# Kernel tuning notes

Measured on AMD Instinct MI355X. Metric: run time of the kernel, lower is better.

The kernel has to match this reference:

```python
import jax, jax.numpy as jnp
import numpy as np

B, H, W, C = 4, 128, 128, 256
HEADS, DHEAD = 8, 32


def conv2d(x, w, b=None, groups=1, pad=0):
    # x: [N,C,H,W], w: [O, C//groups, kh, kw]
    out = jax.lax.conv_general_dilated(
        x, w, window_strides=(1, 1), padding=[(pad, pad), (pad, pad)],
        dimension_numbers=("NCHW", "OIHW", "NCHW"), feature_group_count=groups)
    if b is not None:
        out = out + b[None, :, None, None]
    return out


def setup_inputs() -> dict:
    key = jax.random.key(0)
    ks = jax.random.split(key, 16)
    g = lambda i, shape, s=0.02: jax.random.normal(ks[i], shape, jnp.float32) * s
    return {
        "x": jax.random.normal(ks[0], (B, H, W, C), jnp.float32),
        "mask": jax.random.uniform(ks[1], (1, C, H, W), jnp.float32),
        "wq": g(2, (C, C)),
        "wk": g(3, (C, C)),
        "wv": g(4, (C, C)),
        "rescale": jnp.ones((HEADS, 1, 1), jnp.float32),
        "wproj": g(5, (C, C)),
        "bproj": jnp.zeros((C,), jnp.float32),
        "mg_w1": g(6, (C, C, 1, 1)),
        "mg_b1": jnp.zeros((C,), jnp.float32),
        "mg_w2": g(7, (C, C, 1, 1)),
        "mg_b2": jnp.zeros((C,), jnp.float32),
        "mg_dw": g(8, (C, 1, 5, 5)),
        "mg_db": jnp.zeros((C,), jnp.float32),
        "be_w1": g(9, (C, 1, 3, 3)),
        "be_w2": g(10, (C, 1, 3, 3)),
    }


def _l2norm(t, axis):
    n = jnp.sqrt(jnp.sum(t * t, axis=axis, keepdims=True))
    return t / jnp.maximum(n, 1e-12)


def reference(x, mask, wq, wk, wv, rescale, wproj, bproj,
              mg_w1, mg_b1, mg_w2, mg_b2, mg_dw, mg_db, be_w1, be_w2):
    b, h, w, c = x.shape
    heads = rescale.shape[0]
    d = c // heads
    n = h * w

    xf = x.reshape(b, n, c)
    q_inp = xf @ wq   # [b,n,c]
    k_inp = xf @ wk
    v_inp = xf @ wv

    # MaskGuidedMechanism (h==w so shift_back is identity)
    m = conv2d(mask, mg_w1, mg_b1)                                   # [1,c,h,w]
    attn_map = jax.nn.sigmoid(conv2d(conv2d(m, mg_w2, mg_b2), mg_dw, mg_db, groups=c, pad=2))
    m = m * attn_map + m
    mask_emb = jnp.transpose(m, (0, 2, 3, 1))                        # [1,h,w,c]
    ma = jnp.broadcast_to(mask_emb, (b, h, w, c)).reshape(b, n, c)

    split = lambda t: t.reshape(b, n, heads, d).transpose(0, 2, 1, 3)  # [b,heads,n,d]
    q, k, v, ma = map(split, (q_inp, k_inp, v_inp, ma))
    v = v * ma

    # channel attention: normalize over token dim n
    qn = _l2norm(q, axis=2)
    kn = _l2norm(k, axis=2)
    attn = jnp.einsum("bhni,bhnj->bhij", kn, qn)                     # [b,heads,d,d]
    attn = jax.nn.softmax(attn * rescale, axis=-1)
    out = jnp.einsum("bhij,bhnj->bhin", attn, v)                     # [b,heads,d,n]

    out = out.transpose(0, 3, 1, 2).reshape(b, n, heads * d)         # [b,n,c]
    out_c = (out @ wproj + bproj).reshape(b, h, w, c)

    # band_emb: depthwise3x3 -> GELU(exact) -> depthwise3x3 on v_inp image
    v_img = v_inp.reshape(b, h, w, c).transpose(0, 3, 1, 2)          # [b,c,h,w]
    y = conv2d(v_img, be_w1, groups=c, pad=1)
    y = jax.nn.gelu(y, approximate=False)
    y = conv2d(y, be_w2, groups=c, pad=1)
    out_p = y.transpose(0, 2, 3, 1)

    return out_c + out_p
```

## Files before the change

### kernel.cpp

```cpp
#include <hip/hip_runtime.h>
#include <stdint.h>

#define B 4
#define HW 128
#define C 256
#define NTOK 16384
#define MALL 65536
#define HEADS 8
#define DH 32

typedef float f32x4 __attribute__((ext_vector_type(4)));
typedef short s16x8 __attribute__((ext_vector_type(8)));
typedef short s16x4 __attribute__((ext_vector_type(4)));
typedef __bf16 bf16x8 __attribute__((ext_vector_type(8)));

__device__ __forceinline__ float bf2f(unsigned short u) {
  union { unsigned int i; float f; } x;
  x.i = ((unsigned int)u) << 16;
  return x.f;
}
__device__ __forceinline__ unsigned short f2bf(float f) {
  union { float f; unsigned int i; } x;
  x.f = f;
  unsigned int lsb = (x.i >> 16) & 1u;
  unsigned int r = x.i + 0x7fffu + lsb;
  return (unsigned short)(r >> 16);
}

__device__ __forceinline__ void gload_lds16(const void* g, void* l) {
  auto gp = reinterpret_cast<const __attribute__((address_space(1))) unsigned int*>(
      reinterpret_cast<uintptr_t>(g));
  auto lp = reinterpret_cast<__attribute__((address_space(3))) unsigned int*>(
      reinterpret_cast<uintptr_t>(l));
  __builtin_amdgcn_global_load_lds(gp, lp, 16, 0, 0);
}

#define CFENCE asm volatile("" ::: "memory")
#define RAWBAR()                      \
  do {                                \
    CFENCE;                           \
    __builtin_amdgcn_s_barrier();     \
    CFENCE;                           \
  } while (0)
#define LDSBAR()                                        \
  do {                                                  \
    asm volatile("s_waitcnt lgkmcnt(0)" ::: "memory");  \
    __builtin_amdgcn_s_barrier();                       \
    CFENCE;                                             \
  } while (0)

__global__ __launch_bounds__(256) void cast_x_kernel(const float* __restrict__ x,
                                                     unsigned short* __restrict__ xb) {
  const size_t stride = (size_t)gridDim.x * blockDim.x * 4;
  for (size_t i = ((size_t)blockIdx.x * blockDim.x + threadIdx.x) * 4; i < (size_t)MALL * C;
       i += stride) {
    const float4 v = *(const float4*)&x[i];
    s16x4 o;
    o[0] = (short)f2bf(v.x);
    o[1] = (short)f2bf(v.y);
    o[2] = (short)f2bf(v.z);
    o[3] = (short)f2bf(v.w);
    *(s16x4*)&xb[i] = o;
  }
}

__global__ __launch_bounds__(256) void prep_w_kernel(
    const float* __restrict__ wq, const float* __restrict__ wk, const float* __restrict__ wv,
    const float* __restrict__ wproj, const float* __restrict__ w1, const float* __restrict__ w2,
    unsigned short* __restrict__ wqkvT, unsigned short* __restrict__ wprojT,
    unsigned short* __restrict__ w1b, unsigned short* __restrict__ w2b) {
  const int idx = blockIdx.x * 256 + threadIdx.x;
  const int mat = blockIdx.y;
  const int n = idx >> 8, k = idx & 255;
  switch (mat) {
    case 0: wqkvT[idx] = f2bf(wq[k * 256 + n]); break;
    case 1: wqkvT[65536 + idx] = f2bf(wk[k * 256 + n]); break;
    case 2: wqkvT[131072 + idx] = f2bf(wv[k * 256 + n]); break;
    case 3: wprojT[idx] = f2bf(wproj[k * 256 + n]); break;
    case 4: w1b[idx] = f2bf(w1[idx]); break;
    case 5: w2b[idx] = f2bf(w2[idx]); break;
  }
}

__global__ __launch_bounds__(1024) void tmask_kernel(const float* __restrict__ mask,
                                                     unsigned short* __restrict__ mT) {
  __shared__ float tile[32][33];
  const int p0 = blockIdx.x * 32, c0 = blockIdx.y * 32;
  const int tx = threadIdx.x & 31, ty = threadIdx.x >> 5;
  tile[ty][tx] = mask[(size_t)(c0 + ty) * NTOK + p0 + tx];
  __syncthreads();
  mT[(size_t)(p0 + ty) * C + c0 + tx] = f2bf(tile[tx][ty]);
}

__global__ __launch_bounds__(512) void gemm_bt256_kernel(
    const unsigned short* __restrict__ A, const unsigned short* __restrict__ Bt,
    const int nbn, const int mode, unsigned short* __restrict__ ob0,
    unsigned short* __restrict__ ob1, unsigned short* __restrict__ ob2,
    const float* __restrict__ bias, float* __restrict__ of32,
    const unsigned short* __restrict__ y2) {
  __shared__ alignas(16) unsigned short smem[32768];
  unsigned short* lAb = smem;
  unsigned short* lBb = smem + 16384;
  const int nwg = gridDim.x;
  const int bid = blockIdx.x;
  const int qd = nwg >> 3, rr = nwg & 7;
  const int xcd = bid & 7, sidx = bid >> 3;
  const int swz = (xcd < rr ? xcd * (qd + 1) : rr * (qd + 1) + (xcd - rr) * qd) + sidx;
  const int m0 = (swz / nbn) * 256;
  const int n0 = (swz % nbn) * 256;
  const int t = threadIdx.x;
  const int w = t >> 6, l = t & 63;
  const int wr = w >> 2, wc = w & 3;
  const int lr = l & 15, lg = l >> 4;

  const int srow = t >> 2;
  const int ssl = (t & 3) ^ ((t >> 3) & 3);

  auto stageA = [&](int kt) {
    unsigned short* d = lAb + (kt & 1) * 8192;
    const size_t kb = ((size_t)kt * 32 + ssl * 8) * 2;
    gload_lds16((const char*)A + ((size_t)(m0 + srow) * 256) * 2 + kb, (char*)d + t * 16);
    gload_lds16((const char*)A + ((size_t)(m0 + 128 + srow) * 256) * 2 + kb,
                (char*)d + 8192 + t * 16);
  };
  auto stageB = [&](int kt) {
    unsigned short* d = lBb + (kt & 1) * 8192;
    const size_t kb = ((size_t)kt * 32 + ssl * 8) * 2;
    gload_lds16((const char*)Bt + ((size_t)(n0 + srow) * 256) * 2 + kb, (char*)d + t * 16);
    gload_lds16((const char*)Bt + ((size_t)(n0 + 128 + srow) * 256) * 2 + kb,
                (char*)d + 8192 + t * 16);
  };

  f32x4 acc[8][4];
#pragma unroll
  for (int m = 0; m < 8; ++m)
#pragma unroll
    for (int j = 0; j < 4; ++j) acc[m][j] = f32x4{0.f, 0.f, 0.f, 0.f};

  const int asl = (lg ^ ((lr >> 1) & 3)) * 8;
  const int aoff = lr * 32 + asl;
  const int awb = wr * 4096;
  const int boff = (wc >> 1) * 4096 + ((wc & 1) * 64 + lr) * 32 + asl;

  stageA(0); stageB(0);
  asm volatile("s_waitcnt vmcnt(0)" ::: "memory");
  RAWBAR();

#pragma unroll
  for (int kt = 0; kt < 8; ++kt) {
    const unsigned short* bufA = lAb + (kt & 1) * 8192;
    const unsigned short* bufB = lBb + (kt & 1) * 8192;
    bf16x8 bfr[4], af[4], af2[4];
#pragma unroll
    for (int j = 0; j < 4; ++j) bfr[j] = *(const bf16x8*)&bufB[boff + j * 512];
#pragma unroll
    for (int m = 0; m < 4; ++m) af[m] = *(const bf16x8*)&bufA[awb + aoff + m * 512];
#pragma unroll
    for (int m = 0; m < 4; ++m) af2[m] = *(const bf16x8*)&bufA[awb + aoff + (m + 4) * 512];
    if (kt < 7) { stageA(kt + 1); stageB(kt + 1); }
    __builtin_amdgcn_s_setprio(1);
#pragma unroll
    for (int m = 0; m < 4; ++m)
#pragma unroll
      for (int j = 0; j < 4; ++j)
        acc[m][j] = __builtin_amdgcn_mfma_f32_16x16x32_bf16(af[m], bfr[j], acc[m][j], 0, 0, 0);
#pragma unroll
    for (int m = 0; m < 4; ++m)
#pragma unroll
      for (int j = 0; j < 4; ++j)
        acc[m + 4][j] =
            __builtin_amdgcn_mfma_f32_16x16x32_bf16(af2[m], bfr[j], acc[m + 4][j], 0, 0, 0);
    __builtin_amdgcn_s_setprio(0);
    if (kt < 7) asm volatile("s_waitcnt vmcnt(0)" ::: "memory");
    RAWBAR();
  }

  if (mode == 0) {
    unsigned short* dst = (n0 < 256) ? ob0 : (n0 < 512 ? ob1 : ob2);
    unsigned short* eph = smem;
#pragma unroll
    for (int c = 0; c < 4; ++c) {
      LDSBAR();
      if (wr == (c >> 1)) {
#pragma unroll
        for (int mm = 0; mm < 4; ++mm) {
          const int m = (c & 1) * 4 + mm;
          const int lrow = mm * 16 + lg * 4;
#pragma unroll
          for (int j = 0; j < 4; ++j) {
            const int col = wc * 64 + j * 16 + lr;
#pragma unroll
            for (int r = 0; r < 4; ++r) eph[(lrow + r) * 264 + col] = f2bf(acc[m][j][r]);
          }
        }
      }
      LDSBAR();
      const int col16 = t & 31;
#pragma unroll
      for (int c2 = 0; c2 < 4; ++c2) {
        const int lrow = c2 * 16 + (t >> 5);
        const int grow = m0 + c * 64 + lrow;
        const s16x8 v = *(const s16x8*)&eph[lrow * 264 + col16 * 8];
        *(s16x8*)&dst[(size_t)grow * C + col16 * 8] = v;
      }
    }
  } else {
    float* ephf = (float*)smem;
    const int colc = t & 63;
    const f32x4 bv = *(const f32x4*)&bias[colc * 4];
#pragma unroll
    for (int c = 0; c < 8; ++c) {
      LDSBAR();
      if (wr == (c >> 2)) {
#pragma unroll
        for (int mm = 0; mm < 2; ++mm) {
          const int m = (c & 3) * 2 + mm;
          const int lrow = mm * 16 + lg * 4;
#pragma unroll
          for (int j = 0; j < 4; ++j) {
            const int col = wc * 64 + j * 16 + lr;
#pragma unroll
            for (int r = 0; r < 4; ++r) ephf[(lrow + r) * 260 + col] = acc[m][j][r];
          }
        }
      }
      LDSBAR();
#pragma unroll
      for (int c2 = 0; c2 < 4; ++c2) {
        const int lrow = c2 * 8 + (t >> 6);
        const int grow = m0 + c * 32 + lrow;
        const f32x4 v = *(const f32x4*)&ephf[lrow * 260 + colc * 4];
        const s16x4 yv = *(const s16x4*)&y2[(size_t)grow * C + colc * 4];
        f32x4 o;
#pragma unroll
        for (int e = 0; e < 4; ++e) o[e] = v[e] + bv[e] + bf2f((unsigned short)yv[e]);
        *(f32x4*)&of32[(size_t)grow * C + colc * 4] = o;
      }
    }
  }
}

__global__ __launch_bounds__(256) void gemm_bt_kernel(
    const unsigned short* __restrict__ A, const unsigned short* __restrict__ Bt, const int K,
    const int nbn, const int mode, unsigned short* __restrict__ ob0,
    unsigned short* __restrict__ ob1, unsigned short* __restrict__ ob2,
    const float* __restrict__ bias, float* __restrict__ of32) {
  __shared__ unsigned short lA[2][128 * 64];
  __shared__ unsigned short lB[2][128 * 64];
  const int nwg = gridDim.x;
  const int bid = blockIdx.x;
  const int qd = nwg >> 3, rr = nwg & 7;
  const int xcd = bid & 7, sidx = bid >> 3;
  const int swz = (xcd < rr ? xcd * (qd + 1) : rr * (qd + 1) + (xcd - rr) * qd) + sidx;
  const int m0 = (swz / nbn) * 128;
  const int n0 = (swz % nbn) * 128;
  const int t = threadIdx.x;
  const int w = t >> 6, l = t & 63;
  const int wr = w >> 1, wc = w & 1;
  const int lr = l & 15, lg = l >> 4;

  const int strow = (l >> 3);
  const int scolb = (((l & 7) ^ strow) << 4);

  f32x4 acc[4][4];
#pragma unroll
  for (int i = 0; i < 4; ++i)
#pragma unroll
    for (int j = 0; j < 4; ++j) acc[i][j] = f32x4{0.f, 0.f, 0.f, 0.f};

  auto stage = [&](int buf, int k0) {
#pragma unroll
    for (int s = 0; s < 4; ++s) {
      const int seg = w * 4 + s;
      const int row = seg * 8 + strow;
      gload_lds16((const char*)A + ((size_t)(m0 + row) * K + k0) * 2 + scolb,
                  (char*)&lA[buf][0] + seg * 1024 + (l & 7) * 16);
      gload_lds16((const char*)Bt + ((size_t)(n0 + row) * K + k0) * 2 + scolb,
                  (char*)&lB[buf][0] + seg * 1024 + (l & 7) * 16);
    }
  };
  auto compute = [&](int buf) {
#pragma unroll
    for (int kk = 0; kk < 64; kk += 32) {
      bf16x8 af[4], bfr[4];
      const int sbase = (kk >> 3) + lg;
      const int p = (sbase ^ (lr & 7)) << 3;
#pragma unroll
      for (int i = 0; i < 4; ++i)
        af[i] = *(const bf16x8*)&lA[buf][(wr * 64 + i * 16 + lr) * 64 + p];
#pragma unroll
      for (int j = 0; j < 4; ++j)
        bfr[j] = *(const bf16x8*)&lB[buf][(wc * 64 + j * 16 + lr) * 64 + p];
#pragma unroll
      for (int i = 0; i < 4; ++i)
#pragma unroll
        for (int j = 0; j < 4; ++j)
          acc[i][j] = __builtin_amdgcn_mfma_f32_16x16x32_bf16(af[i], bfr[j], acc[i][j], 0, 0, 0);
    }
  };

  stage(0, 0);
  __syncthreads();
  int cur = 0;
  for (int k0 = 64; k0 < K; k0 += 64) {
    stage(cur ^ 1, k0);
    compute(cur);
    __syncthreads();
    cur ^= 1;
  }
  compute(cur);

#pragma unroll
  for (int i = 0; i < 4; ++i) {
    const int grow = m0 + wr * 64 + i * 16 + lg * 4;
#pragma unroll
    for (int j = 0; j < 4; ++j) {
      const int gcol = n0 + wc * 64 + j * 16 + lr;
#pragma unroll
      for (int r = 0; r < 4; ++r) {
        const float v = acc[i][j][r];
        const size_t row = (size_t)(grow + r);
        if (mode == 0) {
          unsigned short* dst = (gcol < 256) ? ob0 : (gcol < 512 ? ob1 : ob2);
          dst[row * C + (gcol & 255)] = f2bf(v);
        } else if (mode == 1) {
          ob0[row * C + gcol] = f2bf(v + bias[gcol]);
        } else {
          const size_t idx = row * C + gcol;
          of32[idx] += v + bias[gcol];
        }
      }
    }
  }
}

__global__ __launch_bounds__(256) void mask_dw5_kernel(
    const unsigned short* __restrict__ m2, const unsigned short* __restrict__ m1,
    const float* __restrict__ dw, const float* __restrict__ db,
    unsigned short* __restrict__ memb) {
  __shared__ float wlds[25 * 256];
  __shared__ float blds[256];
  const int t = threadIdx.x;
  const int y = blockIdx.y;
  const int x0 = blockIdx.x * 16 + (t >> 6) * 4;
  const int cg = (t & 63) * 4;
#pragma unroll
  for (int e = 0; e < 25; ++e) wlds[e * 256 + t] = dw[t * 25 + e];
  blds[t] = db[t];
  __syncthreads();

  const f32x4 bias = *(const f32x4*)&blds[cg];
  f32x4 acc[4];
#pragma unroll
  for (int xi = 0; xi < 4; ++xi) acc[xi] = bias;

#pragma unroll
  for (int dy = 0; dy < 5; ++dy) {
    const int yy = y + dy - 2;
    if (yy < 0 || yy >= HW) continue;
    f32x4 col[8];
#pragma unroll
    for (int j = 0; j < 8; ++j) {
      const int xx = x0 - 2 + j;
      if (xx >= 0 && xx < HW) {
        const s16x4 v = *(const s16x4*)&m2[((size_t)yy * HW + xx) * C + cg];
        col[j][0] = bf2f((unsigned short)v[0]);
        col[j][1] = bf2f((unsigned short)v[1]);
        col[j][2] = bf2f((unsigned short)v[2]);
        col[j][3] = bf2f((unsigned short)v[3]);
      } else {
        col[j] = f32x4{0.f, 0.f, 0.f, 0.f};
      }
    }
#pragma unroll
    for (int dx = 0; dx < 5; ++dx) {
      const f32x4 wv = *(const f32x4*)&wlds[(dy * 5 + dx) * 256 + cg];
#pragma unroll
      for (int xi = 0; xi < 4; ++xi) acc[xi] += wv * col[dx + xi];
    }
  }

#pragma unroll
  for (int xi = 0; xi < 4; ++xi) {
    const size_t oi = ((size_t)y * HW + x0 + xi) * C + cg;
    const s16x4 mv = *(const s16x4*)&m1[oi];
    s16x4 o;
#pragma unroll
    for (int ch = 0; ch < 4; ++ch) {
      const float a = 1.f / (1.f + __expf(-acc[xi][ch]));
      o[ch] = (short)f2bf(bf2f((unsigned short)mv[ch]) * (1.f + a));
    }
    *(s16x4*)&memb[oi] = o;
  }
}

__global__ __launch_bounds__(256) void gram_kernel(const unsigned short* __restrict__ qb,
                                                   const unsigned short* __restrict__ kb,
                                                   float* __restrict__ Gpart,
                                                   float* __restrict__ ssq,
                                                   float* __restrict__ ssk) {
  const int chunk = blockIdx.x;
  const int h = blockIdx.y;
  const int b = blockIdx.z;
  __shared__ unsigned short lk[128 * 32], lq[128 * 32];
  const int t = threadIdx.x;
  const int wv = t >> 6;
  const int i0 = (t & 7) * 4, j0 = ((t >> 3) & 7) * 4;
  const int lrow = t >> 2, lcb = (t & 3) * 8;
  float acc[4][4] = {};
  float sq[8] = {}, sk[8] = {};
  for (int sub = 0; sub < 8; ++sub) {
    const size_t nbase = (size_t)b * NTOK + chunk * 1024 + sub * 128;
    __syncthreads();
#pragma unroll
    for (int it = 0; it < 2; ++it) {
      const int row = it * 64 + lrow;
      const s16x8 kv8 = *(const s16x8*)&kb[(nbase + row) * C + h * 32 + lcb];
      const s16x8 qv8 = *(const s16x8*)&qb[(nbase + row) * C + h * 32 + lcb];
      *(s16x8*)&lk[row * 32 + lcb] = kv8;
      *(s16x8*)&lq[row * 32 + lcb] = qv8;
#pragma unroll
      for (int e = 0; e < 8; ++e) {
        const float kf = bf2f((unsigned short)kv8[e]);
        sk[e] += kf * kf;
        const float qf = bf2f((unsigned short)qv8[e]);
        sq[e] += qf * qf;
      }
    }
    __syncthreads();
    for (int n = wv; n < 128; n += 4) {
      s16x4 kv = *(const s16x4*)&lk[n * 32 + i0];
      s16x4 qv = *(const s16x4*)&lq[n * 32 + j0];
      float kf[4], qf[4];
#pragma unroll
      for (int e = 0; e < 4; ++e) {
        kf[e] = bf2f((unsigned short)kv[e]);
        qf[e] = bf2f((unsigned short)qv[e]);
      }
#pragma unroll
      for (int a = 0; a < 4; ++a)
#pragma unroll
        for (int bb = 0; bb < 4; ++bb) acc[a][bb] += kf[a] * qf[bb];
    }
  }
  const int pc = chunk * 4 + wv;
  float* dst = Gpart + (((size_t)pc * B + b) * HEADS + h) * 1024;
#pragma unroll
  for (int a = 0; a < 4; ++a)
#pragma unroll
    for (int bb = 0; bb < 4; ++bb) dst[(i0 + a) * 32 + (j0 + bb)] = acc[a][bb];
  __syncthreads();
  float* fq = (float*)lq;
  float* fk = (float*)lk;
#pragma unroll
  for (int e = 0; e < 8; ++e) {
    fq[t * 8 + e] = sq[e];
    fk[t * 8 + e] = sk[e];
  }
  __syncthreads();
  if (t < 32) {
    const int tm = t >> 3, e = t & 7;
    float s1 = 0.f, s2 = 0.f;
    for (int k2 = 0; k2 < 64; ++k2) {
      const int tt = tm + k2 * 4;
      s1 += fq[tt * 8 + e];
      s2 += fk[tt * 8 + e];
    }
    ssq[((size_t)b * 16 + chunk) * C + h * 32 + t] = s1;
    ssk[((size_t)b * 16 + chunk) * C + h * 32 + t] = s2;
  }
}

__global__ __launch_bounds__(256) void softmax_kernel(
    const float* __restrict__ Gpart, const float* __restrict__ ssq,
    const float* __restrict__ ssk, const float* __restrict__ rescale,
    unsigned short* __restrict__ attnb) {
  const int h = blockIdx.x, b = blockIdx.y;
  const int t = threadIdx.x;
  __shared__ float G[1024];
  __shared__ float nq[32], nk[32];
#pragma unroll
  for (int e = 0; e < 4; ++e) {
    const int cell = e * 256 + t;
    float s = 0.f;
    for (int pc = 0; pc < 64; ++pc)
      s += Gpart[(((size_t)pc * B + b) * HEADS + h) * 1024 + cell];
    G[cell] = s;
  }
  if (t < 64) {
    const int d = t & 31;
    const float* ss = (t < 32) ? ssq : ssk;
    float s = 0.f;
    for (int ch = 0; ch < 16; ++ch) s += ss[((size_t)b * 16 + ch) * C + h * 32 + d];
    const float nn = fmaxf(sqrtf(s), 1e-12f);
    if (t < 32) nq[d] = nn;
    else nk[d] = nn;
  }
  __syncthreads();
  if (t < 32) {
    const int i = t;
    const float rs = rescale[h];
    float row[32];
    float mx = -1e30f;
#pragma unroll
    for (int j = 0; j < 32; ++j) {
      const float v = G[i * 32 + j] / (nk[i] * nq[j]) * rs;
      row[j] = v;
      mx = fmaxf(mx, v);
    }
    float sum = 0.f;
#pragma unroll
    for (int j = 0; j < 32; ++j) {
      const float e = expf(row[j] - mx);
      row[j] = e;
      sum += e;
    }
    const float inv = 1.f / sum;
#pragma unroll
    for (int j = 0; j < 32; ++j)
      attnb[(((size_t)b * HEADS + h) * 32 + i) * 32 + j] = f2bf(row[j] * inv);
  }
}

#define PVP 264
#define ATP 40
__global__ __launch_bounds__(256) void pv_kernel(const unsigned short* __restrict__ vb,
                                                 const unsigned short* __restrict__ memb,
                                                 const unsigned short* __restrict__ attnb,
                                                 unsigned short* __restrict__ outp) {
  const int n0 = blockIdx.x * 64;
  const int b = blockIdx.y;
  __shared__ unsigned short vma[64 * PVP];
  __shared__ unsigned short at[HEADS * 32 * ATP];
  const int t = threadIdx.x, w = t >> 6, l = t & 63;
  const int lr = l & 15, lg = l >> 4;
  for (int e = t; e < 8192; e += 256) {
    const int h = e >> 10, ij = e & 1023;
    at[(h * 32 + (ij >> 5)) * ATP + (ij & 31)] = attnb[(size_t)b * 8192 + e];
  }
  {
    const int row = t >> 2, cs = (t & 3) * 64;
#pragma unroll
    for (int i2 = 0; i2 < 8; ++i2) {
      const int c = cs + i2 * 8;
      s16x8 vv = *(const s16x8*)&vb[((size_t)b * NTOK + n0 + row) * C + c];
      s16x8 mm = *(const s16x8*)&memb[(size_t)(n0 + row) * C + c];
      s16x8 o;
#pragma unroll
      for (int e = 0; e < 8; ++e)
        o[e] = (short)f2bf(bf2f((unsigned short)vv[e]) * bf2f((unsigned short)mm[e]));
      *(s16x8*)&vma[row * PVP + c] = o;
    }
  }
  __syncthreads();
  f32x4 acc[4][4];
#pragma unroll
  for (int i = 0; i < 4; ++i)
#pragma unroll
    for (int j = 0; j < 4; ++j) acc[i][j] = f32x4{0.f, 0.f, 0.f, 0.f};
#pragma unroll
  for (int j = 0; j < 4; ++j) {
    const int head = w * 2 + (j >> 1);
    const int colh = (j & 1) * 16 + lr;
    const bf16x8 bfr = *(const bf16x8*)&at[(head * 32 + colh) * ATP + lg * 8];
#pragma unroll
    for (int i = 0; i < 4; ++i) {
      const bf16x8 af = *(const bf16x8*)&vma[(i * 16 + lr) * PVP + head * 32 + lg * 8];
      acc[i][j] = __builtin_amdgcn_mfma_f32_16x16x32_bf16(af, bfr, acc[i][j], 0, 0, 0);
    }
  }
#pragma unroll
  for (int i = 0; i < 4; ++i) {
#pragma unroll
    for (int j = 0; j < 4; ++j) {
      const int head = w * 2 + (j >> 1);
      const int gcol = head * 32 + (j & 1) * 16 + lr;
      const int grow = n0 + i * 16 + lg * 4;
#pragma unroll
      for (int r = 0; r < 4; ++r)
        outp[((size_t)b * NTOK + grow + r) * C + gcol] = f2bf(acc[i][j][r]);
    }
  }
}

__global__ __launch_bounds__(512) void dw3_kernel(const unsigned short* __restrict__ in,
                                                  const float* __restrict__ wgt,
                                                  unsigned short* __restrict__ out_bf,
                                                  float* __restrict__ out_f32,
                                                  const int do_gelu, const int write_f32) {
  const int y = blockIdx.x;
  const int b = blockIdx.y;
  const int t = threadIdx.x;
  const int cg = (t & 63) * 4;
  const int x0 = (t >> 6) * 16;
  float w[9][4];
#pragma unroll
  for (int e = 0; e < 9; ++e)
#pragma unroll
    for (int ch = 0; ch < 4; ++ch) w[e][ch] = wgt[(cg + ch) * 9 + e];
  const int ym = y - 1, yp = y + 1;
  const bool hm = (ym >= 0), hp = (yp < HW);
  const size_t base = (size_t)b * NTOK * C + cg;
  auto ld4 = [&](int yy, int xx) -> f32x4 {
    const s16x4 v = *(const s16x4*)&in[base + ((size_t)yy * HW + xx) * C];
    f32x4 f;
    f[0] = bf2f((unsigned short)v[0]);
    f[1] = bf2f((unsigned short)v[1]);
    f[2] = bf2f((unsigned short)v[2]);
    f[3] = bf2f((unsigned short)v[3]);
    return f;
  };
  const f32x4 zero = {0.f, 0.f, 0.f, 0.f};
  f32x4 a0, a1, a2, b0, b1, b2;
  if (x0 > 0) {
    a0 = hm ? ld4(ym, x0 - 1) : zero;
    a1 = ld4(y, x0 - 1);
    a2 = hp ? ld4(yp, x0 - 1) : zero;
  } else {
    a0 = a1 = a2 = zero;
  }
  b0 = hm ? ld4(ym, x0) : zero;
  b1 = ld4(y, x0);
  b2 = hp ? ld4(yp, x0) : zero;
  for (int xi = 0; xi < 16; ++xi) {
    const int x = x0 + xi;
    f32x4 c0, c1, c2;
    if (x + 1 < HW) {
      c0 = hm ? ld4(ym, x + 1) : zero;
      c1 = ld4(y, x + 1);
      c2 = hp ? ld4(yp, x + 1) : zero;
    } else {
      c0 = c1 = c2 = zero;
    }
    float res[4];
#pragma unroll
    for (int ch = 0; ch < 4; ++ch) {
      float r = w[0][ch] * a0[ch] + w[1][ch] * b0[ch] + w[2][ch] * c0[ch] +
                w[3][ch] * a1[ch] + w[4][ch] * b1[ch] + w[5][ch] * c1[ch] +
                w[6][ch] * a2[ch] + w[7][ch] * b2[ch] + w[8][ch] * c2[ch];
      if (do_gelu) r = 0.5f * r * (1.f + erff(r * 0.70710678118654752f));
      res[ch] = r;
    }
    const size_t oi = base + ((size_t)y * HW + x) * C;
    if (write_f32) {
      const f32x4 o = {res[0], res[1], res[2], res[3]};
      *(f32x4*)&out_f32[oi] = o;
    } else {
      s16x4 o;
      o[0] = (short)f2bf(res[0]);
      o[1] = (short)f2bf(res[1]);
      o[2] = (short)f2bf(res[2]);
      o[3] = (short)f2bf(res[3]);
      *(s16x4*)&out_bf[oi] = o;
    }
    a0 = b0; a1 = b1; a2 = b2;
    b0 = c0; b1 = c1; b2 = c2;
  }
}

extern "C" void kernel_launch(void* const* d_in, const int* in_sizes, int n_in, void* d_out,
                              int out_size, void* d_ws, size_t ws_size, hipStream_t stream) {
  (void)in_sizes; (void)n_in; (void)out_size; (void)ws_size;
  const float* x = (const float*)d_in[0];
  const float* maskp = (const float*)d_in[1];
  const float* wq = (const float*)d_in[2];
  const float* wk = (const float*)d_in[3];
  const float* wv = (const float*)d_in[4];
  const float* rescale = (const float*)d_in[5];
  const float* wproj = (const float*)d_in[6];
  const float* bproj = (const float*)d_in[7];
  const float* mg_w1 = (const float*)d_in[8];
  const float* mg_b1 = (const float*)d_in[9];
  const float* mg_w2 = (const float*)d_in[10];
  const float* mg_b2 = (const float*)d_in[11];
  const float* mg_dw = (const float*)d_in[12];
  const float* mg_db = (const float*)d_in[13];
  const float* be_w1 = (const float*)d_in[14];
  const float* be_w2 = (const float*)d_in[15];
  float* out = (float*)d_out;
  char* ws = (char*)d_ws;

  unsigned short* xb = (unsigned short*)(ws + 0ull);
  unsigned short* qb = (unsigned short*)(ws + 33554432ull);
  unsigned short* kb = (unsigned short*)(ws + 67108864ull);
  unsigned short* vb = (unsigned short*)(ws + 100663296ull);
  unsigned short* mT = (unsigned short*)(ws + 134217728ull);
  unsigned short* m1b = (unsigned short*)(ws + 142606336ull);
  unsigned short* m2b = (unsigned short*)(ws + 150994944ull);
  unsigned short* wqkvT = (unsigned short*)(ws + 159383552ull);
  unsigned short* wprojT = (unsigned short*)(ws + 159776768ull);
  unsigned short* w1b = (unsigned short*)(ws + 159907840ull);
  unsigned short* w2b = (unsigned short*)(ws + 160038912ull);
  float* ssq = (float*)(ws + 160169984ull);
  float* ssk = (float*)(ws + 160432128ull);
  unsigned short* attnb = (unsigned short*)(ws + 160694272ull);
  float* Gpart = (float*)m2b;
  unsigned short* memb = mT;
  unsigned short* outpre = xb;
  unsigned short* y1 = qb;
  unsigned short* y2 = kb;

  cast_x_kernel<<<2048, 256, 0, stream>>>(x, xb);
  prep_w_kernel<<<dim3(256, 6), 256, 0, stream>>>(wq, wk, wv, wproj, mg_w1, mg_w2, wqkvT,
                                                  wprojT, w1b, w2b);
  tmask_kernel<<<dim3(512, 8), 1024, 0, stream>>>(maskp, mT);
  gemm_bt_kernel<<<256, 256, 0, stream>>>(mT, w1b, 256, 2, 1, m1b, nullptr, nullptr, mg_b1,
                                          nullptr);
  gemm_bt_kernel<<<256, 256, 0, stream>>>(m1b, w2b, 256, 2, 1, m2b, nullptr, nullptr, mg_b2,
                                          nullptr);
  mask_dw5_kernel<<<dim3(8, 128), 256, 0, stream>>>(m2b, m1b, mg_dw, mg_db, memb);
  gemm_bt256_kernel<<<768, 512, 0, stream>>>(xb, wqkvT, 3, 0, qb, kb, vb, nullptr, nullptr,
                                             nullptr);
  gram_kernel<<<dim3(16, 8, 4), 256, 0, stream>>>(qb, kb, Gpart, ssq, ssk);
  softmax_kernel<<<dim3(8, 4), 256, 0, stream>>>(Gpart, ssq, ssk, rescale, attnb);
  pv_kernel<<<dim3(256, 4), 256, 0, stream>>>(vb, memb, attnb, outpre);
  dw3_kernel<<<dim3(128, 4), 512, 0, stream>>>(vb, be_w1, y1, nullptr, 1, 0);
  dw3_kernel<<<dim3(128, 4), 512, 0, stream>>>(y1, be_w2, y2, nullptr, 0, 0);
  gemm_bt256_kernel<<<256, 512, 0, stream>>>(outpre, wprojT, 1, 2, nullptr, nullptr, nullptr,
                                             bproj, out, y2);
}
```

Before: 298.4 us.

## Fold attention matrix into projection weights per batch, drop PV kernel

```diff
diff --git a/kernel.cpp b/kernel.cpp
--- a/kernel.cpp
+++ b/kernel.cpp
@@ -108,6 +108,7 @@
   const int swz = (xcd < rr ? xcd * (qd + 1) : rr * (qd + 1) + (xcd - rr) * qd) + sidx;
   const int m0 = (swz / nbn) * 256;
   const int n0 = (swz % nbn) * 256;
+  if (mode == 2) Bt += (size_t)(m0 >> 14) * 65536;
   const int t = threadIdx.x;
   const int w = t >> 6, l = t & 63;
   const int wr = w >> 2, wc = w & 3;
@@ -150,6 +151,7 @@
   for (int kt = 0; kt < 8; ++kt) {
     const unsigned short* bufA = lAb + (kt & 1) * 8192;
     const unsigned short* bufB = lBb + (kt & 1) * 8192;
+    if (kt < 7) { stageA(kt + 1); stageB(kt + 1); }
     bf16x8 bfr[4], af[4], af2[4];
 #pragma unroll
     for (int j = 0; j < 4; ++j) bfr[j] = *(const bf16x8*)&bufB[boff + j * 512];
@@ -157,7 +159,6 @@
     for (int m = 0; m < 4; ++m) af[m] = *(const bf16x8*)&bufA[awb + aoff + m * 512];
 #pragma unroll
     for (int m = 0; m < 4; ++m) af2[m] = *(const bf16x8*)&bufA[awb + aoff + (m + 4) * 512];
-    if (kt < 7) { stageA(kt + 1); stageB(kt + 1); }
     __builtin_amdgcn_s_setprio(1);
 #pragma unroll
     for (int m = 0; m < 4; ++m)
@@ -402,7 +403,7 @@
   const int chunk = blockIdx.x;
   const int h = blockIdx.y;
   const int b = blockIdx.z;
-  __shared__ unsigned short lk[128 * 32], lq[128 * 32];
+  __shared__ float flk[128 * 32], flq[128 * 32];
   const int t = threadIdx.x;
   const int wv = t >> 6;
   const int i0 = (t & 7) * 4, j0 = ((t >> 3) & 7) * 4;
@@ -417,30 +418,34 @@
       const int row = it * 64 + lrow;
       const s16x8 kv8 = *(const s16x8*)&kb[(nbase + row) * C + h * 32 + lcb];
       const s16x8 qv8 = *(const s16x8*)&qb[(nbase + row) * C + h * 32 + lcb];
-      *(s16x8*)&lk[row * 32 + lcb] = kv8;
-      *(s16x8*)&lq[row * 32 + lcb] = qv8;
-#pragma unroll
-      for (int e = 0; e < 8; ++e) {
-        const float kf = bf2f((unsigned short)kv8[e]);
-        sk[e] += kf * kf;
-        const float qf = bf2f((unsigned short)qv8[e]);
-        sq[e] += qf * qf;
-      }
+      f32x4 ka, kbb, qa, qbb;
+#pragma unroll
+      for (int e = 0; e < 4; ++e) {
+        ka[e] = bf2f((unsigned short)kv8[e]);
+        kbb[e] = bf2f((unsigned short)kv8[e + 4]);
+        qa[e] = bf2f((unsigned short)qv8[e]);
+        qbb[e] = bf2f((unsigned short)qv8[e + 4]);
+      }
+#pragma unroll
+      for (int e = 0; e < 4; ++e) {
+        sk[e] += ka[e] * ka[e];
+        sk[e + 4] += kbb[e] * kbb[e];
+        sq[e] += qa[e] * qa[e];
+        sq[e + 4] += qbb[e] * qbb[e];
+      }
+      *(f32x4*)&flk[row * 32 + lcb] = ka;
+      *(f32x4*)&flk[row * 32 + lcb + 4] = kbb;
+      *(f32x4*)&flq[row * 32 + lcb] = qa;
+      *(f32x4*)&flq[row * 32 + lcb + 4] = qbb;
     }
     __syncthreads();
     for (int n = wv; n < 128; n += 4) {
-      s16x4 kv = *(const s16x4*)&lk[n * 32 + i0];
-      s16x4 qv = *(const s16x4*)&lq[n * 32 + j0];
-      float kf[4], qf[4];
-#pragma unroll
-      for (int e = 0; e < 4; ++e) {
-        kf[e] = bf2f((unsigned short)kv[e]);
-        qf[e] = bf2f((unsigned short)qv[e]);
-      }
+      const f32x4 kv = *(const f32x4*)&flk[n * 32 + i0];
+      const f32x4 qv = *(const f32x4*)&flq[n * 32 + j0];
 #pragma unroll
       for (int a = 0; a < 4; ++a)
 #pragma unroll
-        for (int bb = 0; bb < 4; ++bb) acc[a][bb] += kf[a] * qf[bb];
+        for (int bb = 0; bb < 4; ++bb) acc[a][bb] += kv[a] * qv[bb];
     }
   }
   const int pc = chunk * 4 + wv;
@@ -450,12 +455,10 @@
 #pragma unroll
     for (int bb = 0; bb < 4; ++bb) dst[(i0 + a) * 32 + (j0 + bb)] = acc[a][bb];
   __syncthreads();
-  float* fq = (float*)lq;
-  float* fk = (float*)lk;
 #pragma unroll
   for (int e = 0; e < 8; ++e) {
-    fq[t * 8 + e] = sq[e];
-    fk[t * 8 + e] = sk[e];
+    flq[t * 8 + e] = sq[e];
+    flk[t * 8 + e] = sk[e];
   }
   __syncthreads();
   if (t < 32) {
@@ -463,8 +466,8 @@
     float s1 = 0.f, s2 = 0.f;
     for (int k2 = 0; k2 < 64; ++k2) {
       const int tt = tm + k2 * 4;
-      s1 += fq[tt * 8 + e];
-      s2 += fk[tt * 8 + e];
+      s1 += flq[tt * 8 + e];
+      s2 += flk[tt * 8 + e];
     }
     ssq[((size_t)b * 16 + chunk) * C + h * 32 + t] = s1;
     ssk[((size_t)b * 16 + chunk) * C + h * 32 + t] = s2;
@@ -522,64 +525,51 @@
   }
 }
 
-#define PVP 264
-#define ATP 40
-__global__ __launch_bounds__(256) void pv_kernel(const unsigned short* __restrict__ vb,
-                                                 const unsigned short* __restrict__ memb,
-                                                 const unsigned short* __restrict__ attnb,
-                                                 unsigned short* __restrict__ outp) {
-  const int n0 = blockIdx.x * 64;
+__global__ __launch_bounds__(256) void weff_kernel(const unsigned short* __restrict__ attnb,
+                                                   const unsigned short* __restrict__ wprojT,
+                                                   unsigned short* __restrict__ weff) {
   const int b = blockIdx.y;
-  __shared__ unsigned short vma[64 * PVP];
-  __shared__ unsigned short at[HEADS * 32 * ATP];
-  const int t = threadIdx.x, w = t >> 6, l = t & 63;
-  const int lr = l & 15, lg = l >> 4;
-  for (int e = t; e < 8192; e += 256) {
-    const int h = e >> 10, ij = e & 1023;
-    at[(h * 32 + (ij >> 5)) * ATP + (ij & 31)] = attnb[(size_t)b * 8192 + e];
-  }
-  {
-    const int row = t >> 2, cs = (t & 3) * 64;
-#pragma unroll
-    for (int i2 = 0; i2 < 8; ++i2) {
-      const int c = cs + i2 * 8;
-      s16x8 vv = *(const s16x8*)&vb[((size_t)b * NTOK + n0 + row) * C + c];
-      s16x8 mm = *(const s16x8*)&memb[(size_t)(n0 + row) * C + c];
-      s16x8 o;
-#pragma unroll
-      for (int e = 0; e < 8; ++e)
-        o[e] = (short)f2bf(bf2f((unsigned short)vv[e]) * bf2f((unsigned short)mm[e]));
-      *(s16x8*)&vma[row * PVP + c] = o;
-    }
-  }
+  const int co0 = blockIdx.x * 64;
+  const int t = threadIdx.x;
+  __shared__ float att[8192];
+  for (int e = t; e < 8192; e += 256) att[e] = bf2f(attnb[(size_t)b * 8192 + e]);
   __syncthreads();
-  f32x4 acc[4][4];
-#pragma unroll
-  for (int i = 0; i < 4; ++i)
-#pragma unroll
-    for (int j = 0; j < 4; ++j) acc[i][j] = f32x4{0.f, 0.f, 0.f, 0.f};
-#pragma unroll
-  for (int j = 0; j < 4; ++j) {
-    const int head = w * 2 + (j >> 1);
-    const int colh = (j & 1) * 16 + lr;
-    const bf16x8 bfr = *(const bf16x8*)&at[(head * 32 + colh) * ATP + lg * 8];
-#pragma unroll
-    for (int i = 0; i < 4; ++i) {
-      const bf16x8 af = *(const bf16x8*)&vma[(i * 16 + lr) * PVP + head * 32 + lg * 8];
-      acc[i][j] = __builtin_amdgcn_mfma_f32_16x16x32_bf16(af, bfr, acc[i][j], 0, 0, 0);
-    }
-  }
-#pragma unroll
-  for (int i = 0; i < 4; ++i) {
-#pragma unroll
-    for (int j = 0; j < 4; ++j) {
-      const int head = w * 2 + (j >> 1);
-      const int gcol = head * 32 + (j & 1) * 16 + lr;
-      const int grow = n0 + i * 16 + lg * 4;
-#pragma unroll
-      for (int r = 0; r < 4; ++r)
-        outp[((size_t)b * NTOK + grow + r) * C + gcol] = f2bf(acc[i][j][r]);
-    }
+  const int o = co0 + (t & 63);
+  const int hq = t >> 6;
+#pragma unroll
+  for (int hh = 0; hh < 2; ++hh) {
+    const int h = hq * 2 + hh;
+    float wp[32];
+#pragma unroll
+    for (int i = 0; i < 32; ++i) wp[i] = bf2f(wprojT[(size_t)o * 256 + h * 32 + i]);
+    for (int j4 = 0; j4 < 8; ++j4) {
+      f32x4 s = {0.f, 0.f, 0.f, 0.f};
+#pragma unroll
+      for (int i = 0; i < 32; ++i) {
+        const f32x4 a4 = *(const f32x4*)&att[(h * 32 + i) * 32 + j4 * 4];
+        s += wp[i] * a4;
+      }
+      s16x4 oo;
+#pragma unroll
+      for (int e = 0; e < 4; ++e) oo[e] = (short)f2bf(s[e]);
+      *(s16x4*)&weff[((size_t)b * 256 + o) * 256 + h * 32 + j4 * 4] = oo;
+    }
+  }
+}
+
+__global__ __launch_bounds__(256) void vma_kernel(const unsigned short* __restrict__ vb,
+                                                  const unsigned short* __restrict__ memb,
+                                                  unsigned short* __restrict__ vma) {
+  const size_t n8 = (size_t)MALL * C / 8;
+  const size_t stride = (size_t)gridDim.x * blockDim.x;
+  for (size_t i8 = (size_t)blockIdx.x * blockDim.x + threadIdx.x; i8 < n8; i8 += stride) {
+    const s16x8 vv = *(const s16x8*)&vb[i8 * 8];
+    const s16x8 mm = *(const s16x8*)&memb[(i8 & ((size_t)NTOK * C / 8 - 1)) * 8];
+    s16x8 o;
+#pragma unroll
+    for (int e = 0; e < 8; ++e)
+      o[e] = (short)f2bf(bf2f((unsigned short)vv[e]) * bf2f((unsigned short)mm[e]));
+    *(s16x8*)&vma[i8 * 8] = o;
   }
 }
 
@@ -696,9 +686,10 @@
   unsigned short* attnb = (unsigned short*)(ws + 160694272ull);
   float* Gpart = (float*)m2b;
   unsigned short* memb = mT;
-  unsigned short* outpre = xb;
+  unsigned short* vma = xb;
   unsigned short* y1 = qb;
   unsigned short* y2 = kb;
+  unsigned short* weff = m1b;
 
   cast_x_kernel<<<2048, 256, 0, stream>>>(x, xb);
   prep_w_kernel<<<dim3(256, 6), 256, 0, stream>>>(wq, wk, wv, wproj, mg_w1, mg_w2, wqkvT,
@@ -713,9 +704,10 @@
                                              nullptr);
   gram_kernel<<<dim3(16, 8, 4), 256, 0, stream>>>(qb, kb, Gpart, ssq, ssk);
   softmax_kernel<<<dim3(8, 4), 256, 0, stream>>>(Gpart, ssq, ssk, rescale, attnb);
-  pv_kernel<<<dim3(256, 4), 256, 0, stream>>>(vb, memb, attnb, outpre);
+  weff_kernel<<<dim3(4, 4), 256, 0, stream>>>(attnb, wprojT, weff);
+  vma_kernel<<<2048, 256, 0, stream>>>(vb, memb, vma);
   dw3_kernel<<<dim3(128, 4), 512, 0, stream>>>(vb, be_w1, y1, nullptr, 1, 0);
   dw3_kernel<<<dim3(128, 4), 512, 0, stream>>>(y1, be_w2, y2, nullptr, 0, 0);
-  gemm_bt256_kernel<<<256, 512, 0, stream>>>(outpre, wprojT, 1, 2, nullptr, nullptr, nullptr,
+  gemm_bt256_kernel<<<256, 512, 0, stream>>>(vma, weff, 1, 2, nullptr, nullptr, nullptr,
                                              bproj, out, y2);
 }
```

New measurement: 305.8 us. 2.5% more time.
